# Kernel tuning notes

Measured on AMD Instinct MI355X. Metric: run time of the kernel, lower is better.

The kernel has to match this reference:

```python
import jax, jax.numpy as jnp
import numpy as np

NUM_GROUPS = 32
EPS = 1e-5

def group_norm(x, weight, bias):
    # x: [B, C, H, W]
    b, c, h, w = x.shape
    g = NUM_GROUPS
    xg = x.reshape(b, g, (c // g) * h * w)
    mean = xg.mean(axis=-1, keepdims=True)
    var = xg.var(axis=-1, keepdims=True)
    xn = ((xg - mean) * jax.lax.rsqrt(var + EPS)).reshape(b, c, h, w)
    return xn * weight[None, :, None, None] + bias[None, :, None, None]

def setup_inputs() -> dict:
    key = jax.random.key(0)
    ks = jax.random.split(key, 4)
    B, C, H, W = 4, 256, 64, 64
    x = jax.random.normal(ks[0], (B, C, H, W), dtype=jnp.float32)
    gn_weight = jnp.ones((C,), dtype=jnp.float32)
    gn_bias = jnp.zeros((C,), dtype=jnp.float32)
    # 1x1 conv == linear over channel dim; init ~ kaiming-uniform-ish scale
    qkv_weight = jax.random.normal(ks[1], (3 * C, C), dtype=jnp.float32) / np.sqrt(C)
    qkv_bias = jnp.zeros((3 * C,), dtype=jnp.float32)
    out_weight = jax.random.normal(ks[2], (C, C), dtype=jnp.float32) / np.sqrt(C)
    out_bias = jnp.zeros((C,), dtype=jnp.float32)
    return {"x": x, "gn_weight": gn_weight, "gn_bias": gn_bias,
            "qkv_weight": qkv_weight, "qkv_bias": qkv_bias,
            "out_weight": out_weight, "out_bias": out_bias}

def reference(x, gn_weight, gn_bias, qkv_weight, qkv_bias, out_weight, out_bias):
    b, c, h, w = x.shape
    n = h * w
    xn = group_norm(x, gn_weight, gn_bias)
    # 1x1 conv QKV projection: [B, 3C, H, W]
    qkv = jnp.einsum('bchw,oc->bohw', xn, qkv_weight) + qkv_bias[None, :, None, None]
    q, k, v = jnp.split(qkv, 3, axis=1)
    q = q.transpose(0, 2, 3, 1).reshape(b, n, c)   # [B, N, C]
    k = k.reshape(b, c, n)                         # [B, C, N]
    v = v.transpose(0, 2, 3, 1).reshape(b, n, c)   # [B, N, C]
    scores = jnp.einsum('bnc,bcm->bnm', q, k) * (c ** -0.5)  # [B, N, N]
    attn = jax.nn.softmax(scores, axis=-1)
    out = jnp.einsum('bnm,bmc->bnc', attn, v)      # [B, N, C]
    out = out.reshape(b, h, w, c).transpose(0, 3, 1, 2)  # [B, C, H, W]
    out = jnp.einsum('bchw,oc->bohw', out, out_weight) + out_bias[None, :, None, None]
    return out + x
```

## Files before the change

kernel.cpp:

```cpp
#include <hip/hip_runtime.h>
#include <math.h>

#define B_   4
#define C_   256
#define G_   32
#define CPG  8
#define N_   4096
#define NPG  (CPG * N_)
#define EPS  1e-5f
#define SCALE 0.0625f
#define NCH  32

typedef __attribute__((ext_vector_type(8)))  __bf16 bf16x8;
typedef __attribute__((ext_vector_type(4)))  __bf16 bf16x4;
typedef __attribute__((ext_vector_type(16))) float  f32x16;

__device__ __forceinline__ void stage16(const __bf16* g, __bf16* l) {
    __builtin_amdgcn_global_load_lds(
        (const __attribute__((address_space(1))) unsigned int*)g,
        (__attribute__((address_space(3))) unsigned int*)l, 16, 0, 0);
}

__global__ __launch_bounds__(256) void gn_stats_kernel(const float* __restrict__ x,
                                                       float* __restrict__ part) {
    int bid = blockIdx.x;
    int bg = bid >> 2, seg = bid & 3;
    const float4* xp4 = (const float4*)(x + (size_t)bg * NPG) + seg * 2048;
    int tid = threadIdx.x;

    float s = 0.f, ss = 0.f;
    for (int i = tid; i < 2048; i += 256) {
        float4 t = xp4[i];
        s  += t.x + t.y + t.z + t.w;
        ss += t.x * t.x + t.y * t.y + t.z * t.z + t.w * t.w;
    }
    #pragma unroll
    for (int off = 32; off; off >>= 1) {
        s  += __shfl_xor(s, off, 64);
        ss += __shfl_xor(ss, off, 64);
    }
    __shared__ float rs[2][4];
    int wave = tid >> 6, lane = tid & 63;
    if (lane == 0) { rs[0][wave] = s; rs[1][wave] = ss; }
    __syncthreads();
    if (tid == 0) {
        part[bid * 2]     = rs[0][0] + rs[0][1] + rs[0][2] + rs[0][3];
        part[bid * 2 + 1] = rs[1][0] + rs[1][1] + rs[1][2] + rs[1][3];
    }
}

__global__ __launch_bounds__(256) void gn_apply_kernel(const float* __restrict__ x,
                                                       const float* __restrict__ w,
                                                       const float* __restrict__ bia,
                                                       const float* __restrict__ part,
                                                       __bf16* __restrict__ xnb) {
    int bid = blockIdx.x;
    int b   = (bid & 7) >> 1;
    int u   = ((bid >> 3) << 1) | (bid & 1);
    int g   = u >> 2;
    int seg = u & 3;
    int bg  = b * 32 + g;
    float s  = part[(bg * 4 + 0) * 2] + part[(bg * 4 + 1) * 2]
             + part[(bg * 4 + 2) * 2] + part[(bg * 4 + 3) * 2];
    float ss = part[(bg * 4 + 0) * 2 + 1] + part[(bg * 4 + 1) * 2 + 1]
             + part[(bg * 4 + 2) * 2 + 1] + part[(bg * 4 + 3) * 2 + 1];
    float mean = s / (float)NPG;
    float var  = ss / (float)NPG - mean * mean;
    float rstd = rsqrtf(var + EPS);

    const float* xp = x + (size_t)bg * NPG;
    int n0 = seg * 1024 + threadIdx.x * 4;

    float4 t[8];
    #pragma unroll
    for (int cc = 0; cc < 8; cc++)
        t[cc] = *(const float4*)(xp + (size_t)cc * N_ + n0);

    float sc[8], sh[8];
    #pragma unroll
    for (int cc = 0; cc < 8; cc++) {
        sc[cc] = rstd * w[g * CPG + cc];
        sh[cc] = bia[g * CPG + cc] - mean * sc[cc];
    }

    size_t base = ((((size_t)(b * 128 + (n0 >> 5)) * 16 + (g >> 1)) * 2 + (g & 1))
                   * 32 + (n0 & 31)) * 8;
    #pragma unroll
    for (int j = 0; j < 4; j++) {
        bf16x8 pk;
        #pragma unroll
        for (int cc = 0; cc < 8; cc++) {
            float tv = ((const float*)&t[cc])[j];
            pk[cc] = (__bf16)(tv * sc[cc] + sh[cc]);
        }
        *(bf16x8*)(xnb + base + j * 8) = pk;
    }
}

__global__ __launch_bounds__(256) void qkv_kernel(const __bf16* __restrict__ xnb,
                                                  const float* __restrict__ W,
                                                  const float* __restrict__ bias,
                                                  __bf16* __restrict__ q,
                                                  __bf16* __restrict__ k,
                                                  __bf16* __restrict__ v) {
    __shared__ __align__(16) __bf16 x_lds[2][8192];
    int bid = blockIdx.x;
    int b   = (bid & 7) >> 1;
    int t2  = ((bid >> 3) << 1) | (bid & 1);
    int ot  = t2 >> 5;
    int nc  = t2 & 31;
    int tid = threadIdx.x, wv = tid >> 6, lane = tid & 63;
    int n31 = lane & 31, q2 = lane >> 5;
    int B0 = ot * 128 + wv * 32;

    bf16x8 wf[16];
    const float* wp = W + (size_t)(B0 + n31) * C_;
    #pragma unroll
    for (int ks = 0; ks < 16; ks++) {
        float4 t0 = *(const float4*)(wp + ks * 16 + q2 * 8);
        float4 t1 = *(const float4*)(wp + ks * 16 + q2 * 8 + 4);
        bf16x8 f;
        f[0] = (__bf16)t0.x; f[1] = (__bf16)t0.y; f[2] = (__bf16)t0.z; f[3] = (__bf16)t0.w;
        f[4] = (__bf16)t1.x; f[5] = (__bf16)t1.y; f[6] = (__bf16)t1.z; f[7] = (__bf16)t1.w;
        wf[ks] = f;
    }

    float bv[16], bvv = 0.f;
    if (ot < 4) {
        #pragma unroll
        for (int gI = 0; gI < 4; gI++)
            #pragma unroll
            for (int j = 0; j < 4; j++)
                bv[gI * 4 + j] = bias[B0 + gI * 8 + 4 * q2 + j];
    } else {
        bvv = bias[B0 + n31];
    }

    const __bf16* xb = xnb + (size_t)b * 128 * 8192;
    const __bf16* xgs = xb + (size_t)(nc * 4) * 8192 + wv * 2048 + lane * 8;

    {
        __bf16* l = (__bf16*)x_lds[0] + wv * 2048;
        #pragma unroll
        for (int i = 0; i < 4; i++)
            stage16(xgs + i * 512, l + i * 512);
    }

    for (int t = 0; t < 4; t++) {
        __syncthreads();
        if (t < 3) {
            const __bf16* g_ = xgs + (size_t)(t + 1) * 8192;
            __bf16* l = (__bf16*)x_lds[(t + 1) & 1] + wv * 2048;
            #pragma unroll
            for (int i = 0; i < 4; i++)
                stage16(g_ + i * 512, l + i * 512);
        }
        int nt = nc * 4 + t;
        const __bf16* xl = (const __bf16*)x_lds[t & 1] + q2 * 256 + n31 * 8;
        bf16x8 xf[16];
        #pragma unroll
        for (int ks = 0; ks < 16; ks++) xf[ks] = *(const bf16x8*)(xl + ks * 512);

        f32x16 acc;
        #pragma unroll
        for (int i = 0; i < 16; i++) acc[i] = 0.f;
        if (ot < 4) {
            #pragma unroll
            for (int ks = 0; ks < 16; ks++)
                acc = __builtin_amdgcn_mfma_f32_32x32x16_bf16(wf[ks], xf[ks], acc, 0, 0, 0);
        } else {
            #pragma unroll
            for (int ks = 0; ks < 16; ks++)
                acc = __builtin_amdgcn_mfma_f32_32x32x16_bf16(xf[ks], wf[ks], acc, 0, 0, 0);
        }

        if (ot < 4) {
            int ocb = (ot < 2) ? B0 : (B0 - 256);
            __bf16* dst = (ot < 2) ? q : k;
            bool isq = (ot < 2);
            #pragma unroll
            for (int gI = 0; gI < 4; gI++) {
                bf16x4 pk;
                #pragma unroll
                for (int j = 0; j < 4; j++) {
                    float y = acc[gI * 4 + j] + bv[gI * 4 + j];
                    if (isq) y *= SCALE;
                    pk[j] = (__bf16)y;
                }
                size_t idx = ((((size_t)(b * 128 + nt) * 16 + ((ocb >> 4) + (gI >> 1))) * 2
                               + (gI & 1)) * 32 + n31) * 8 + 4 * q2;
                *(bf16x4*)(dst + idx) = pk;
            }
        } else {
            int ocb = B0 - 512;
            #pragma unroll
            for (int gI = 0; gI < 4; gI++) {
                bf16x4 pk;
                #pragma unroll
                for (int j = 0; j < 4; j++)
                    pk[j] = (__bf16)(acc[gI * 4 + j] + bvv);
                size_t idx = (((((size_t)(b * 128 + nt) * 2 + (gI >> 1)) * 2 + (gI & 1)) * 8
                               + (ocb >> 5)) * 32 + n31) * 8 + 4 * q2;
                *(bf16x4*)(v + idx) = pk;
            }
        }
    }
}

__global__ __launch_bounds__(512, 4) void attn_kernel(const __bf16* __restrict__ q,
                                                      const __bf16* __restrict__ k,
                                                      const __bf16* __restrict__ v,
                                                      __bf16* __restrict__ aob,
                                                      float* __restrict__ lpart,
                                                      float* __restrict__ ltmp) {
    __shared__ __align__(16) __bf16 k_lds[2][16384];
    __shared__ __align__(16) __bf16 p_lds[2][64 * 64];

    int bid   = blockIdx.x;
    int xcd   = bid & 7;
    int b     = xcd >> 1;
    int split = xcd & 1;
    int qt    = bid >> 3;
    int n0    = qt * 64;

    int tid = threadIdx.x;
    int wid = tid >> 6, lane = tid & 63;
    int n31 = lane & 31, q2 = lane >> 5;

    const size_t BSTR = (size_t)N_ * C_;
    const size_t PLANE = (size_t)B_ * C_ * N_;
    float* lt = ltmp + (size_t)bid * 128;
    const __bf16* kgbase = k + (size_t)(b * 128 + split * 64) * 8192
                           + wid * 2048 + lane * 8;

    {
        __bf16* l = (__bf16*)k_lds[0] + wid * 2048;
        #pragma unroll
        for (int i = 0; i < 4; i++)
            stage16(kgbase + i * 512, l + i * 512);
    }

    if (wid < 4) {
        int kt = wid & 1;
        int rt = wid >> 1;
        const __bf16* qg = q + (size_t)(b * 128 + qt * 2 + rt) * 8192
                           + q2 * 256 + n31 * 8;
        bf16x8 qf[16];
        #pragma unroll
        for (int ks = 0; ks < 16; ks++) qf[ks] = *(const bf16x8*)(qg + ks * 512);

        float l_acc = 0.f;
        int prow = rt * 32 + n31;
        int swz  = (prow & 7) << 4;
        int klo  = kt * 8192 + q2 * 256 + n31 * 8;

        for (int ch = 0; ch < NCH; ch++) {
            __syncthreads();
            if (ch < NCH - 1) {
                const __bf16* g = kgbase + (size_t)(ch + 1) * 16384;
                __bf16* l = (__bf16*)k_lds[(ch + 1) & 1] + wid * 2048;
                #pragma unroll
                for (int i = 0; i < 4; i++)
                    stage16(g + i * 512, l + i * 512);
            }
            const __bf16* kl = (const __bf16*)k_lds[ch & 1] + klo;
            f32x16 sa, sb;
            #pragma unroll
            for (int i = 0; i < 16; i++) { sa[i] = 0.f; sb[i] = 0.f; }
            __builtin_amdgcn_s_setprio(1);
            #pragma unroll
            for (int i = 0; i < 8; i++) {
                bf16x8 ka = *(const bf16x8*)(kl + i * 512);
                bf16x8 kb = *(const bf16x8*)(kl + (i + 8) * 512);
                sa = __builtin_amdgcn_mfma_f32_32x32x16_bf16(ka, qf[i], sa, 0, 0, 0);
                sb = __builtin_amdgcn_mfma_f32_32x32x16_bf16(kb, qf[i + 8], sb, 0, 0, 0);
            }
            __builtin_amdgcn_s_setprio(0);
            char* pbuf = (char*)p_lds[ch & 1];
            #pragma unroll
            for (int gI = 0; gI < 4; gI++) {
                bf16x4 pw;
                #pragma unroll
                for (int j = 0; j < 4; j++) {
                    float p = __expf(sa[gI * 4 + j] + sb[gI * 4 + j]);
                    l_acc += p;
                    pw[j] = (__bf16)p;
                }
                int off = prow * 128 + kt * 64 + 16 * gI + 8 * q2;
                *(bf16x4*)(pbuf + (off ^ swz)) = pw;
            }
        }
        l_acc += __shfl_down(l_acc, 32);
        if (lane < 32) lt[kt * 64 + rt * 32 + lane] = l_acc;
        __syncthreads();
    } else {
        int cw = wid - 4;
        const __bf16* vbase = v + (size_t)b * BSTR + (size_t)split * 524288
                              + (size_t)q2 * 2048 + n31 * 8;
        f32x16 o_acc[2][2];
        #pragma unroll
        for (int ct = 0; ct < 2; ct++)
            #pragma unroll
            for (int rt = 0; rt < 2; rt++)
                #pragma unroll
                for (int i = 0; i < 16; i++) o_acc[ct][rt][i] = 0.f;

        for (int ch = 0; ch < NCH; ch++) {
            __syncthreads();
            if (ch < NCH - 1) {
                const __bf16* g = kgbase + (size_t)(ch + 1) * 16384;
                __bf16* l = (__bf16*)k_lds[(ch + 1) & 1] + wid * 2048;
                #pragma unroll
                for (int i = 0; i < 4; i++)
                    stage16(g + i * 512, l + i * 512);
            }
            if (ch > 0) {
                int cc = ch - 1;
                bf16x8 vf[2][4];
                #pragma unroll
                for (int ct = 0; ct < 2; ct++)
                    #pragma unroll
                    for (int ks4 = 0; ks4 < 4; ks4++) {
                        size_t off = (size_t)(cc * 2 + (ks4 >> 1)) * 8192
                                   + (size_t)(ks4 & 1) * 4096 + (cw * 2 + ct) * 256;
                        vf[ct][ks4] = *(const bf16x8*)(vbase + off);
                    }
                const char* pbuf = (const char*)p_lds[cc & 1];
                __builtin_amdgcn_s_setprio(1);
                #pragma unroll
                for (int rt = 0; rt < 2; rt++) {
                    int prow = rt * 32 + n31;
                    int swz  = (prow & 7) << 4;
                    int pbs  = prow * 128 + q2 * 16;
                    #pragma unroll
                    for (int ks4 = 0; ks4 < 4; ks4++) {
                        bf16x8 pf = *(const bf16x8*)(pbuf + ((pbs + ks4 * 32) ^ swz));
                        o_acc[0][rt] = __builtin_amdgcn_mfma_f32_32x32x16_bf16(
                            vf[0][ks4], pf, o_acc[0][rt], 0, 0, 0);
                        o_acc[1][rt] = __builtin_amdgcn_mfma_f32_32x32x16_bf16(
                            vf[1][ks4], pf, o_acc[1][rt], 0, 0, 0);
                    }
                }
                __builtin_amdgcn_s_setprio(0);
            }
        }
        __syncthreads();
        float lA = lt[n31] + lt[64 + n31];
        float lB = lt[32 + n31] + lt[64 + 32 + n31];
        {
            int cc = NCH - 1;
            bf16x8 vf[2][4];
            #pragma unroll
            for (int ct = 0; ct < 2; ct++)
                #pragma unroll
                for (int ks4 = 0; ks4 < 4; ks4++) {
                    size_t off = (size_t)(cc * 2 + (ks4 >> 1)) * 8192
                               + (size_t)(ks4 & 1) * 4096 + (cw * 2 + ct) * 256;
                    vf[ct][ks4] = *(const bf16x8*)(vbase + off);
                }
            const char* pbuf = (const char*)p_lds[1];
            __builtin_amdgcn_s_setprio(1);
            #pragma unroll
            for (int rt = 0; rt < 2; rt++) {
                int prow = rt * 32 + n31;
                int swz  = (prow & 7) << 4;
                int pbs  = prow * 128 + q2 * 16;
                #pragma unroll
                for (int ks4 = 0; ks4 < 4; ks4++) {
                    bf16x8 pf = *(const bf16x8*)(pbuf + ((pbs + ks4 * 32) ^ swz));
                    o_acc[0][rt] = __builtin_amdgcn_mfma_f32_32x32x16_bf16(
                        vf[0][ks4], pf, o_acc[0][rt], 0, 0, 0);
                    o_acc[1][rt] = __builtin_amdgcn_mfma_f32_32x32x16_bf16(
                        vf[1][ks4], pf, o_acc[1][rt], 0, 0, 0);
                }
            }
            __builtin_amdgcn_s_setprio(0);
        }
        if (wid == 4 && lane < 32) {
            float* lp = lpart + ((size_t)split * B_ + b) * N_ + n0;
            lp[n31]      = lA;
            lp[32 + n31] = lB;
        }
        float inv0 = 1.0f / lA;
        float inv1 = 1.0f / lB;
        __bf16* aop = aob + (size_t)split * PLANE;
        #pragma unroll
        for (int ct = 0; ct < 2; ct++)
            #pragma unroll
            for (int rt = 0; rt < 2; rt++) {
                float inv = rt ? inv1 : inv0;
                #pragma unroll
                for (int g = 0; g < 4; g++) {
                    bf16x4 st;
                    #pragma unroll
                    for (int j = 0; j < 4; j++)
                        st[j] = (__bf16)(o_acc[ct][rt][g * 4 + j] * inv);
                    size_t idx = ((((((size_t)(b * 64 + qt) * 4 + cw) * 2 + ct) * 2 + rt)
                                   * 4 + g) * 2 + q2) * 128 + n31 * 4;
                    *(bf16x4*)(aop + idx) = st;
                }
            }
    }
}

__global__ __launch_bounds__(256) void proj_kernel(const __bf16* __restrict__ aob,
                                                   const float* __restrict__ lpart,
                                                   const float* __restrict__ W2,
                                                   const float* __restrict__ bias,
                                                   const float* __restrict__ x,
                                                   float* __restrict__ out) {
    int bid = blockIdx.x;
    int b   = (bid & 7) >> 1;
    int u   = ((bid >> 3) << 1) | (bid & 1);
    int ot  = u >> 6;
    int tp  = u & 63;
    int tid = threadIdx.x, wv = tid >> 6, lane = tid & 63;
    int n31 = lane & 31, q2 = lane >> 5;
    int B0 = ot * 128 + wv * 32;
    const size_t BN = (size_t)B_ * N_;
    const size_t PLANE = (size_t)B_ * C_ * N_;

    bf16x8 wf[16];
    const float* wp = W2 + (size_t)(B0 + n31) * C_;
    #pragma unroll
    for (int ks = 0; ks < 16; ks++) {
        float4 t0 = *(const float4*)(wp + ks * 16 + q2 * 8);
        float4 t1 = *(const float4*)(wp + ks * 16 + q2 * 8 + 4);
        bf16x8 f;
        f[0] = (__bf16)t0.x; f[1] = (__bf16)t0.y; f[2] = (__bf16)t0.z; f[3] = (__bf16)t0.w;
        f[4] = (__bf16)t1.x; f[5] = (__bf16)t1.y; f[6] = (__bf16)t1.z; f[7] = (__bf16)t1.w;
        wf[ks] = f;
    }
    float bv[16];
    #pragma unroll
    for (int r = 0; r < 16; r++) bv[r] = bias[B0 + (r & 3) + 8 * (r >> 2) + 4 * q2];

    for (int t = 0; t < 2; t++) {
        int nt = tp * 2 + t;
        int qt = nt >> 1, rtile = nt & 1;
        int n = nt * 32 + n31;
        size_t ln = (size_t)b * N_ + n;
        float l0v = lpart[ln];
        float l1v = lpart[BN + ln];
        float invt = 1.0f / (l0v + l1v);
        float w0 = l0v * invt, w1 = l1v * invt;

        bf16x8 xf[16];
        #pragma unroll
        for (int ks = 0; ks < 16; ks++) {
            int oct = ks * 2 + q2;
            int cw = oct >> 3, ct = (oct >> 2) & 1, ga = oct & 3;
            size_t base = ((((((size_t)(b * 64 + qt) * 4 + cw) * 2 + ct) * 2 + rtile)
                            * 4 + ga) * 2) * 128 + n31 * 4;
            bf16x4 a0 = *(const bf16x4*)(aob + base);
            bf16x4 b0 = *(const bf16x4*)(aob + base + 128);
            bf16x4 a1 = *(const bf16x4*)(aob + PLANE + base);
            bf16x4 b1 = *(const bf16x4*)(aob + PLANE + base + 128);
            bf16x8 f;
            #pragma unroll
            for (int j = 0; j < 4; j++) {
                f[j]     = (__bf16)(w0 * (float)a0[j] + w1 * (float)a1[j]);
                f[4 + j] = (__bf16)(w0 * (float)b0[j] + w1 * (float)b1[j]);
            }
            xf[ks] = f;
        }

        f32x16 acc;
        #pragma unroll
        for (int i = 0; i < 16; i++) acc[i] = 0.f;
        #pragma unroll
        for (int ks = 0; ks < 16; ks++)
            acc = __builtin_amdgcn_mfma_f32_32x32x16_bf16(wf[ks], xf[ks], acc, 0, 0, 0);

        #pragma unroll
        for (int r = 0; r < 16; r++) {
            int o = B0 + (r & 3) + 8 * (r >> 2) + 4 * q2;
            size_t idx = ((size_t)(b * C_ + o)) * N_ + nt * 32 + n31;
            out[idx] = acc[r] + bv[r] + x[idx];
        }
    }
}

extern "C" void kernel_launch(void* const* d_in, const int* in_sizes, int n_in,
                              void* d_out, int out_size, void* d_ws, size_t ws_size,
                              hipStream_t stream) {
    const float* x     = (const float*)d_in[0];
    const float* gn_w  = (const float*)d_in[1];
    const float* gn_b  = (const float*)d_in[2];
    const float* qkv_w = (const float*)d_in[3];
    const float* qkv_b = (const float*)d_in[4];
    const float* out_w = (const float*)d_in[5];
    const float* out_b = (const float*)d_in[6];
    float* out = (float*)d_out;

    const size_t SZ = (size_t)B_ * C_ * N_;
    char* base = (char*)d_ws;
    __bf16* aob = (__bf16*)base;
    __bf16* xnb = (__bf16*)base;
    __bf16* qb  = (__bf16*)(base + 2 * SZ * 4);
    __bf16* kb  = qb + SZ;
    __bf16* vb  = kb + SZ;
    float*  lpart = (float*)(base + 2 * SZ * 4 + 3 * SZ * 2);
    float*  part  = lpart + 2 * (size_t)B_ * N_;
    float*  ltmp  = part + 1024;

    gn_stats_kernel<<<dim3(512), 256, 0, stream>>>(x, part);
    gn_apply_kernel<<<dim3(512), 256, 0, stream>>>(x, gn_w, gn_b, part, xnb);
    qkv_kernel<<<dim3(768), 256, 0, stream>>>(xnb, qkv_w, qkv_b, qb, kb, vb);
    attn_kernel<<<dim3(512), 512, 0, stream>>>(qb, kb, vb, aob, lpart, ltmp);
    proj_kernel<<<dim3(512), 256, 0, stream>>>(aob, lpart, out_w, out_b, x, out);
}
```

Baseline: 205.0 us.

## Pre-convert weights to bf16 once and restructure QKV to loop over outputs

Extra blocks in the stats kernel convert the QKV and output-projection weights to bf16 in workspace. Both GEMM kernels then load bf16 weights directly instead of reconverting fp32 per block. The QKV kernel now stages one spatial tile of normalized activations once and loops over all six output tiles, reading weights from cache. This drops the double-buffered pipeline and cuts the grid from 768 to 512 blocks, which may expose weight-load latency inside the loop.

```diff
diff --git a/kernel.cpp b/kernel.cpp
--- a/kernel.cpp
+++ b/kernel.cpp
@@ -10,6 +10,8 @@
 #define EPS  1e-5f
 #define SCALE 0.0625f
 #define NCH  32
+#define QKVW_ELEMS 196608
+#define OUTW_ELEMS 65536
 
 typedef __attribute__((ext_vector_type(8)))  __bf16 bf16x8;
 typedef __attribute__((ext_vector_type(4)))  __bf16 bf16x4;
@@ -22,8 +24,27 @@
 }
 
 __global__ __launch_bounds__(256) void gn_stats_kernel(const float* __restrict__ x,
-                                                       float* __restrict__ part) {
+                                                       float* __restrict__ part,
+                                                       const float* __restrict__ qw,
+                                                       const float* __restrict__ ow,
+                                                       __bf16* __restrict__ wqb,
+                                                       __bf16* __restrict__ wob) {
     int bid = blockIdx.x;
+    if (bid >= 512) {
+        int et = (bid - 512) * 256 + threadIdx.x;
+        int e8 = et * 8;
+        const float* src;
+        __bf16* dst;
+        if (e8 < QKVW_ELEMS) { src = qw + e8; dst = wqb + e8; }
+        else { src = ow + (e8 - QKVW_ELEMS); dst = wob + (e8 - QKVW_ELEMS); }
+        float4 t0 = *(const float4*)src;
+        float4 t1 = *(const float4*)(src + 4);
+        bf16x8 f;
+        f[0] = (__bf16)t0.x; f[1] = (__bf16)t0.y; f[2] = (__bf16)t0.z; f[3] = (__bf16)t0.w;
+        f[4] = (__bf16)t1.x; f[5] = (__bf16)t1.y; f[6] = (__bf16)t1.z; f[7] = (__bf16)t1.w;
+        *(bf16x8*)dst = f;
+        return;
+    }
     int bg = bid >> 2, seg = bid & 3;
     const float4* xp4 = (const float4*)(x + (size_t)bg * NPG) + seg * 2048;
     int tid = threadIdx.x;
@@ -98,68 +119,41 @@
 }
 
 __global__ __launch_bounds__(256) void qkv_kernel(const __bf16* __restrict__ xnb,
-                                                  const float* __restrict__ W,
+                                                  const __bf16* __restrict__ Wb,
                                                   const float* __restrict__ bias,
                                                   __bf16* __restrict__ q,
                                                   __bf16* __restrict__ k,
                                                   __bf16* __restrict__ v) {
-    __shared__ __align__(16) __bf16 x_lds[2][8192];
+    __shared__ __align__(16) __bf16 x_lds[8192];
     int bid = blockIdx.x;
     int b   = (bid & 7) >> 1;
-    int t2  = ((bid >> 3) << 1) | (bid & 1);
-    int ot  = t2 >> 5;
-    int nc  = t2 & 31;
+    int nt  = ((bid >> 3) << 1) | (bid & 1);
     int tid = threadIdx.x, wv = tid >> 6, lane = tid & 63;
     int n31 = lane & 31, q2 = lane >> 5;
-    int B0 = ot * 128 + wv * 32;
-
-    bf16x8 wf[16];
-    const float* wp = W + (size_t)(B0 + n31) * C_;
-    #pragma unroll
-    for (int ks = 0; ks < 16; ks++) {
-        float4 t0 = *(const float4*)(wp + ks * 16 + q2 * 8);
-        float4 t1 = *(const float4*)(wp + ks * 16 + q2 * 8 + 4);
-        bf16x8 f;
-        f[0] = (__bf16)t0.x; f[1] = (__bf16)t0.y; f[2] = (__bf16)t0.z; f[3] = (__bf16)t0.w;
-        f[4] = (__bf16)t1.x; f[5] = (__bf16)t1.y; f[6] = (__bf16)t1.z; f[7] = (__bf16)t1.w;
-        wf[ks] = f;
-    }
-
-    float bv[16], bvv = 0.f;
-    if (ot < 4) {
-        #pragma unroll
-        for (int gI = 0; gI < 4; gI++)
-            #pragma unroll
-            for (int j = 0; j < 4; j++)
-                bv[gI * 4 + j] = bias[B0 + gI * 8 + 4 * q2 + j];
-    } else {
-        bvv = bias[B0 + n31];
-    }
-
-    const __bf16* xb = xnb + (size_t)b * 128 * 8192;
-    const __bf16* xgs = xb + (size_t)(nc * 4) * 8192 + wv * 2048 + lane * 8;
-
+
+    const __bf16* xgs = xnb + (size_t)b * 1048576 + (size_t)nt * 8192
+                        + wv * 2048 + lane * 8;
     {
-        __bf16* l = (__bf16*)x_lds[0] + wv * 2048;
+        __bf16* l = x_lds + wv * 2048;
         #pragma unroll
         for (int i = 0; i < 4; i++)
             stage16(xgs + i * 512, l + i * 512);
     }
-
-    for (int t = 0; t < 4; t++) {
-        __syncthreads();
-        if (t < 3) {
-            const __bf16* g_ = xgs + (size_t)(t + 1) * 8192;
-            __bf16* l = (__bf16*)x_lds[(t + 1) & 1] + wv * 2048;
-            #pragma unroll
-            for (int i = 0; i < 4; i++)
-                stage16(g_ + i * 512, l + i * 512);
-        }
-        int nt = nc * 4 + t;
-        const __bf16* xl = (const __bf16*)x_lds[t & 1] + q2 * 256 + n31 * 8;
-        bf16x8 xf[16];
-        #pragma unroll
-        for (int ks = 0; ks < 16; ks++) xf[ks] = *(const bf16x8*)(xl + ks * 512);
+    __syncthreads();
+
+    bf16x8 xf[16];
+    const __bf16* xl = x_lds + q2 * 256 + n31 * 8;
+    #pragma unroll
+    for (int ks = 0; ks < 16; ks++) xf[ks] = *(const bf16x8*)(xl + ks * 512);
+
+    #pragma unroll 1
+    for (int ot = 0; ot < 6; ot++) {
+        int B0 = ot * 128 + wv * 32;
+        bf16x8 wf[16];
+        const __bf16* wp = Wb + (size_t)(B0 + n31) * C_;
+        #pragma unroll
+        for (int ks = 0; ks < 16; ks++)
+            wf[ks] = *(const bf16x8*)(wp + ks * 16 + q2 * 8);
 
         f32x16 acc;
         #pragma unroll
@@ -183,7 +177,7 @@
                 bf16x4 pk;
                 #pragma unroll
                 for (int j = 0; j < 4; j++) {
-                    float y = acc[gI * 4 + j] + bv[gI * 4 + j];
+                    float y = acc[gI * 4 + j] + bias[B0 + gI * 8 + 4 * q2 + j];
                     if (isq) y *= SCALE;
                     pk[j] = (__bf16)y;
                 }
@@ -193,6 +187,7 @@
             }
         } else {
             int ocb = B0 - 512;
+            float bvv = bias[B0 + n31];
             #pragma unroll
             for (int gI = 0; gI < 4; gI++) {
                 bf16x4 pk;
@@ -405,7 +400,7 @@
 
 __global__ __launch_bounds__(256) void proj_kernel(const __bf16* __restrict__ aob,
                                                    const float* __restrict__ lpart,
-                                                   const float* __restrict__ W2,
+                                                   const __bf16* __restrict__ W2b,
                                                    const float* __restrict__ bias,
                                                    const float* __restrict__ x,
                                                    float* __restrict__ out) {
@@ -421,16 +416,10 @@
     const size_t PLANE = (size_t)B_ * C_ * N_;
 
     bf16x8 wf[16];
-    const float* wp = W2 + (size_t)(B0 + n31) * C_;
-    #pragma unroll
-    for (int ks = 0; ks < 16; ks++) {
-        float4 t0 = *(const float4*)(wp + ks * 16 + q2 * 8);
-        float4 t1 = *(const float4*)(wp + ks * 16 + q2 * 8 + 4);
-        bf16x8 f;
-        f[0] = (__bf16)t0.x; f[1] = (__bf16)t0.y; f[2] = (__bf16)t0.z; f[3] = (__bf16)t0.w;
-        f[4] = (__bf16)t1.x; f[5] = (__bf16)t1.y; f[6] = (__bf16)t1.z; f[7] = (__bf16)t1.w;
-        wf[ks] = f;
-    }
+    const __bf16* wp = W2b + (size_t)(B0 + n31) * C_;
+    #pragma unroll
+    for (int ks = 0; ks < 16; ks++)
+        wf[ks] = *(const bf16x8*)(wp + ks * 16 + q2 * 8);
     float bv[16];
     #pragma unroll
     for (int r = 0; r < 16; r++) bv[r] = bias[B0 + (r & 3) + 8 * (r >> 2) + 4 * q2];
@@ -502,11 +491,13 @@
     __bf16* vb  = kb + SZ;
     float*  lpart = (float*)(base + 2 * SZ * 4 + 3 * SZ * 2);
     float*  part  = lpart + 2 * (size_t)B_ * N_;
-    float*  ltmp  = part + 1024;
-
-    gn_stats_kernel<<<dim3(512), 256, 0, stream>>>(x, part);
+    float*  ltmp  = part + 1536;
+    __bf16* wqb   = (__bf16*)(ltmp + 512 * 128);
+    __bf16* wob   = wqb + QKVW_ELEMS;
+
+    gn_stats_kernel<<<dim3(640), 256, 0, stream>>>(x, part, qkv_w, out_w, wqb, wob);
     gn_apply_kernel<<<dim3(512), 256, 0, stream>>>(x, gn_w, gn_b, part, xnb);
-    qkv_kernel<<<dim3(768), 256, 0, stream>>>(xnb, qkv_w, qkv_b, qb, kb, vb);
+    qkv_kernel<<<dim3(512), 256, 0, stream>>>(xnb, wqb, qkv_b, qb, kb, vb);
     attn_kernel<<<dim3(512), 512, 0, stream>>>(qb, kb, vb, aob, lpart, ltmp);
-    proj_kernel<<<dim3(512), 256, 0, stream>>>(aob, lpart, out_w, out_b, x, out);
-}
+    proj_kernel<<<dim3(512), 256, 0, stream>>>(aob, lpart, wob, out_b, x, out);
+}
```

Result: no change. 205.9 us (+0.5%).
